# Kernel tuning notes

Hardware: AMD Instinct MI355X
Metric: run time of the kernel (lower is better)

## Reference

```python
import jax, jax.numpy as jnp
import numpy as np

N = 100000
E = 3200000
D = 128


def setup_inputs() -> dict:
    key = jax.random.key(0)
    k1, k2, k3, k4 = jax.random.split(key, 4)
    x = jax.random.normal(k1, (N, D), dtype=jnp.float32)
    edge_index = jax.random.randint(k2, (2, E), 0, N, dtype=jnp.int64)
    W1 = jax.random.normal(k3, (D, 16), dtype=jnp.float32) * (1.0 / np.sqrt(D))
    b1 = jnp.zeros((16,), dtype=jnp.float32)
    W2 = jax.random.normal(k4, (16, 2), dtype=jnp.float32) * (1.0 / np.sqrt(16))
    b2 = jnp.zeros((2,), dtype=jnp.float32)
    return {"x": x, "edge_index": edge_index, "W1": W1, "b1": b1, "W2": W2, "b2": b2}


def _gcn_conv(h, src, dst, norm, W, b):
    # transform first (out_dim <= in_dim), then normalized scatter-add aggregation
    h = h @ W                                   # [N, out]
    msg = h[src] * norm[:, None]                # [E+N, out] gathered messages
    agg = jax.ops.segment_sum(msg, dst, num_segments=N)
    return agg + b


def reference(x, edge_index, W1, b1, W2, b2):
    loops = jnp.arange(N, dtype=edge_index.dtype)
    src = jnp.concatenate([edge_index[0], loops])   # row (message source)
    dst = jnp.concatenate([edge_index[1], loops])   # col (aggregation target)
    # symmetric GCN normalization: deg over dst, norm = d^-1/2[src] * d^-1/2[dst]
    deg = jax.ops.segment_sum(jnp.ones_like(src, dtype=x.dtype), dst, num_segments=N)
    dinv = jnp.where(deg > 0, jax.lax.rsqrt(deg), 0.0)
    norm = dinv[src] * dinv[dst]

    h = _gcn_conv(x, src, dst, norm, W1, b1)
    h = jax.nn.relu(h)
    h = _gcn_conv(h, src, dst, norm, W2, b2)
    return jax.nn.log_softmax(h, axis=1)
```

## Files before the change

### kernel.cpp

```cpp
#include <hip/hip_runtime.h>
#include <hip/hip_fp16.h>
#include <math.h>

#define N_NODES 100000
#define N_EDGES 3200000
#define D_IN    128
#define H1      16

#define BSH     8
#define NPB     256
#define NB      391
#define CAP     13056
#define PBLK    512
#define CHUNK   6250
#define ELS_CAP 12128
#define NLINES  (ELS_CAP / 16)
#define MROWS   64
#define SLOTS   26
#define AELS    5120


__global__ __launch_bounds__(512) void k_zero(int* __restrict__ cursor) {
    int t = threadIdx.x;
    if (t < NB) cursor[t] = 0;
}

__global__ __launch_bounds__(512) void k_partition(const int* __restrict__ ei,
                                                   int* __restrict__ cursor,
                                                   unsigned int* __restrict__ eop) {
    __shared__ int h[512];
    __shared__ int loff[512];
    __shared__ int resv[NB];
    __shared__ unsigned short owner[NLINES];
    __shared__ unsigned char rank8[CHUNK];
    __shared__ unsigned int els[ELS_CAP];
    int t = threadIdx.x;
    h[t] = 0;
    __syncthreads();
    int c0 = blockIdx.x * CHUNK;
    const int* srcs = ei + c0;
    const int* dsts = ei + N_EDGES + c0;
    for (int i = t; i < CHUNK; i += 512)
        rank8[i] = (unsigned char)atomicAdd(&h[dsts[i] >> BSH], 1);
    __syncthreads();
    int cp = (h[t] + 15) & ~15;
    loff[t] = cp;
    __syncthreads();
    for (int o = 1; o < 512; o <<= 1) {
        int u = (t >= o) ? loff[t - o] : 0;
        __syncthreads();
        loff[t] += u;
        __syncthreads();
    }
    int inc = loff[t];
    int totalpad = loff[511];
    int ex = inc - cp;
    __syncthreads();
    loff[t] = ex;
    if (t < NB && cp) {
        resv[t] = atomicAdd(&cursor[t], cp);
        int l0 = ex >> 4;
        for (int k = 0; k < (cp >> 4); ++k) owner[l0 + k] = (unsigned short)t;
    }
    for (int i = t; i < totalpad; i += 512) els[i] = 0xFFFFFFFFu;
    __syncthreads();
    for (int i = t; i < CHUNK; i += 512) {
        int s = srcs[i];
        int d = dsts[i];
        int b = d >> BSH;
        els[loff[b] + (int)rank8[i]] = ((unsigned)s << BSH) | (unsigned)(d & (NPB - 1));
    }
    __syncthreads();
    for (int i = t; i < totalpad; i += 512) {
        int b   = owner[i >> 4];
        int pos = resv[b] + (i - loff[b]);
        if (pos < CAP)
            eop[(size_t)b * CAP + pos] = els[i];
    }
}

__global__ __launch_bounds__(512) void k_count(const int* __restrict__ cursor,
                                               const unsigned int* __restrict__ eop,
                                               float* __restrict__ dinv) {
    __shared__ int cnt[128];
    int t = threadIdx.x;
    int b = blockIdx.x >> 1, hh = blockIdx.x & 1;
    if (t < 128) cnt[t] = 0;
    __syncthreads();
    int n = cursor[b]; if (n > CAP) n = CAP;
    const unsigned int* reg = eop + (size_t)b * CAP;
    for (int i = t; i < n; i += 512) {
        unsigned int v = reg[i];
        if ((int)v >= 0) {
            int dloc = v & (NPB - 1);
            if ((dloc >> 7) == hh) atomicAdd(&cnt[dloc & 127], 1);
        }
    }
    __syncthreads();
    if (t < 128) {
        int node = (b << BSH) + (hh << 7) + t;
        if (node < N_NODES) dinv[node] = rsqrtf((float)(cnt[t] + 1));
    }
}

__global__ __launch_bounds__(256) void k_mm1(const float* __restrict__ x,
                                             const float* __restrict__ W1,
                                             const float* __restrict__ dinv,
                                             __half* __restrict__ h1h) {
    __shared__ float sX[MROWS][D_IN + 1];
    int t = threadIdx.x;
    int r0 = blockIdx.x * MROWS;
    for (int i = t; i < MROWS * (D_IN / 4); i += 256) {
        int row = i >> 5, c4 = i & 31;
        int grow = r0 + row;
        float4 v = (grow < N_NODES) ? ((const float4*)x)[(size_t)grow * 32 + c4]
                                    : make_float4(0.f, 0.f, 0.f, 0.f);
        sX[row][c4 * 4 + 0] = v.x; sX[row][c4 * 4 + 1] = v.y;
        sX[row][c4 * 4 + 2] = v.z; sX[row][c4 * 4 + 3] = v.w;
    }
    __syncthreads();
    int lane = t & 63;
    int c0 = __builtin_amdgcn_readfirstlane((t >> 6) * 4);
    float a0 = 0.f, a1 = 0.f, a2 = 0.f, a3 = 0.f;
#pragma unroll 4
    for (int d = 0; d < D_IN; ++d) {
        float xv = sX[lane][d];
        a0 = fmaf(xv, W1[d * 16 + c0 + 0], a0);
        a1 = fmaf(xv, W1[d * 16 + c0 + 1], a1);
        a2 = fmaf(xv, W1[d * 16 + c0 + 2], a2);
        a3 = fmaf(xv, W1[d * 16 + c0 + 3], a3);
    }
    int grow = r0 + lane;
    if (grow < N_NODES) {
        float di = dinv[grow];
        __half2* o = (__half2*)(h1h + (size_t)grow * H1 + c0);
        o[0] = __floats2half2_rn(a0 * di, a1 * di);
        o[1] = __floats2half2_rn(a2 * di, a3 * di);
    }
}

__global__ __launch_bounds__(512) void k_agg1f(const int* __restrict__ cursor,
                                               const unsigned int* __restrict__ eop,
                                               const __half* __restrict__ h1h,
                                               const float* __restrict__ dinv,
                                               const float* __restrict__ b1,
                                               const float* __restrict__ W2,
                                               float2* __restrict__ h2f) {
    __shared__ int cnt[128], off[128];
    __shared__ int els[AELS];
    int t = threadIdx.x;
    int b = blockIdx.x >> 1, hh = blockIdx.x & 1;
    if (t < 128) cnt[t] = 0;
    __syncthreads();
    int n = cursor[b]; if (n > CAP) n = CAP;
    const unsigned int* reg = eop + (size_t)b * CAP;
    unsigned int vals[SLOTS];
#pragma unroll
    for (int k = 0; k < SLOTS; ++k) {
        int i = t + k * 512;
        unsigned int w = 0xFFFFFFFFu;
        if (i < n) {
            unsigned int v = reg[i];
            if ((int)v >= 0) {
                int dloc = v & (NPB - 1);
                if ((dloc >> 7) == hh) {
                    int r = atomicAdd(&cnt[dloc & 127], 1);
                    w = (v >> 8) | ((unsigned)(r & 127) << 17)
                                 | ((unsigned)(dloc & 127) << 24);
                }
            }
        }
        vals[k] = w;
    }
    __syncthreads();
    int val = (t < 128) ? cnt[t] : 0;
    if (t < 128) off[t] = val;
    __syncthreads();
    for (int o = 1; o < 128; o <<= 1) {
        int u = 0;
        if (t < 128 && t >= o) u = off[t - o];
        __syncthreads();
        if (t < 128) off[t] += u;
        __syncthreads();
    }
    if (t < 128) off[t] -= val;
    __syncthreads();
#pragma unroll
    for (int k = 0; k < SLOTS; ++k) {
        unsigned int w = vals[k];
        if (w != 0xFFFFFFFFu) {
            int src  = w & 0x1FFFF;
            int r    = (w >> 17) & 127;
            int dloc = (w >> 24) & 127;
            int p = off[dloc] + r;
            if (p < AELS) els[p] = src;
        }
    }
    __syncthreads();
    int g = t >> 4, l = t & 15;
    for (int nn = g; nn < 128; nn += 32) {
        int node = (b << BSH) + (hh << 7) + nn;
        if (node >= N_NODES) continue;
        int e = cnt[nn], base = off[nn];
        float acc = 0.f;
        int j = 0;
        for (; j + 4 <= e; j += 4) {
            int s0 = els[base + j],     s1 = els[base + j + 1];
            int s2 = els[base + j + 2], s3 = els[base + j + 3];
            acc += __half2float(h1h[s0 * H1 + l]) + __half2float(h1h[s1 * H1 + l])
                 + __half2float(h1h[s2 * H1 + l]) + __half2float(h1h[s3 * H1 + l]);
        }
        for (; j < e; ++j) acc += __half2float(h1h[els[base + j] * H1 + l]);
        float di = dinv[node];
        float s  = acc + __half2float(h1h[node * H1 + l]);
        float h  = fmaxf(fmaf(di, s, b1[l]), 0.f);
        float p0 = h * W2[2 * l], p1 = h * W2[2 * l + 1];
#pragma unroll
        for (int o2 = 1; o2 < 16; o2 <<= 1) {
            p0 += __shfl_xor(p0, o2);
            p1 += __shfl_xor(p1, o2);
        }
        if (l == 0) h2f[node] = make_float2(p0 * di, p1 * di);
    }
}

__global__ __launch_bounds__(512) void k_agg2f(const int* __restrict__ cursor,
                                               const unsigned int* __restrict__ eop,
                                               const float2* __restrict__ h2f,
                                               const float* __restrict__ dinv,
                                               const float* __restrict__ b2,
                                               float* __restrict__ out) {
    __shared__ float ax[128], ay[128];
    int t = threadIdx.x;
    int b = blockIdx.x >> 1, hh = blockIdx.x & 1;
    if (t < 128) { ax[t] = 0.f; ay[t] = 0.f; }
    __syncthreads();
    int n = cursor[b]; if (n > CAP) n = CAP;
    const unsigned int* reg = eop + (size_t)b * CAP;
    for (int i = t; i < n; i += 512) {
        unsigned int v = reg[i];
        if ((int)v >= 0) {
            int dloc = v & (NPB - 1);
            if ((dloc >> 7) == hh) {
                float2 m = h2f[v >> 8];
                atomicAdd(&ax[dloc & 127], m.x);
                atomicAdd(&ay[dloc & 127], m.y);
            }
        }
    }
    __syncthreads();
    if (t < 128) {
        int node = (b << BSH) + (hh << 7) + t;
        if (node < N_NODES) {
            float di = dinv[node];
            float2 self = h2f[node];
            float a0 = fmaf(di, ax[t] + self.x, b2[0]);
            float a1 = fmaf(di, ay[t] + self.y, b2[1]);
            float m  = fmaxf(a0, a1);
            float lg = logf(expf(a0 - m) + expf(a1 - m));
            out[2 * node]     = a0 - m - lg;
            out[2 * node + 1] = a1 - m - lg;
        }
    }
}

extern "C" void kernel_launch(void* const* d_in, const int* in_sizes, int n_in,
                              void* d_out, int out_size, void* d_ws, size_t ws_size,
                              hipStream_t stream) {
    const float* x  = (const float*)d_in[0];
    const int*   ei = (const int*)d_in[1];
    const float* W1 = (const float*)d_in[2];
    const float* b1 = (const float*)d_in[3];
    const float* W2 = (const float*)d_in[4];
    const float* b2 = (const float*)d_in[5];
    float* out = (float*)d_out;

    int*          cursor = (int*)d_ws;
    float*        dinv   = (float*)(cursor + 512);
    __half*       h1h    = (__half*)(dinv + 100352);
    float2*       h2f    = (float2*)(h1h + (size_t)100352 * H1);
    unsigned int* eop    = (unsigned int*)(h2f + 100352);

    k_zero     <<<1,      512, 0, stream>>>(cursor);
    k_partition<<<PBLK,   512, 0, stream>>>(ei, cursor, eop);
    k_count    <<<NB * 2, 512, 0, stream>>>(cursor, eop, dinv);
    k_mm1      <<<(N_NODES + MROWS - 1) / MROWS, 256, 0, stream>>>(x, W1, dinv, h1h);
    k_agg1f    <<<NB * 2, 512, 0, stream>>>(cursor, eop, h1h, dinv, b1, W2, h2f);
    k_agg2f    <<<NB * 2, 512, 0, stream>>>(cursor, eop, h2f, dinv, b2, out);
}
```

Baseline: 248.2 us.

## Precompute per-node CSR offsets in k_count and vectorize edge and feature gathers

k_count now also runs a per-half-bucket prefix scan and writes each node's degree and offset to global buffers. k_agg1f reads these instead of re-counting and re-scanning, scattering sources directly into shared memory through per-node atomic cursors and dropping the 26-slot register staging array. All edge-stream loops read the partitioned edge list as uint4, and layer-1 aggregation uses 4 threads per node, each loading 4 halves at once, instead of 16 threads loading one half each. This adds two global arrays and relies on each bucket's edge count being a multiple of 4.

```diff
diff --git a/kernel.cpp b/kernel.cpp
--- a/kernel.cpp
+++ b/kernel.cpp
@@ -16,9 +16,10 @@
 #define ELS_CAP 12128
 #define NLINES  (ELS_CAP / 16)
 #define MROWS   64
-#define SLOTS   26
 #define AELS    5120
 
+
+union H4 { uint2 u; __half2 h[2]; };
 
 __global__ __launch_bounds__(512) void k_zero(int* __restrict__ cursor) {
     int t = threadIdx.x;
@@ -81,25 +82,39 @@
 
 __global__ __launch_bounds__(512) void k_count(const int* __restrict__ cursor,
                                                const unsigned int* __restrict__ eop,
-                                               float* __restrict__ dinv) {
-    __shared__ int cnt[128];
+                                               float* __restrict__ dinv,
+                                               int* __restrict__ gdeg,
+                                               int* __restrict__ goff) {
+    __shared__ int cnt[128], off[128];
     int t = threadIdx.x;
     int b = blockIdx.x >> 1, hh = blockIdx.x & 1;
     if (t < 128) cnt[t] = 0;
     __syncthreads();
     int n = cursor[b]; if (n > CAP) n = CAP;
-    const unsigned int* reg = eop + (size_t)b * CAP;
-    for (int i = t; i < n; i += 512) {
-        unsigned int v = reg[i];
-        if ((int)v >= 0) {
-            int dloc = v & (NPB - 1);
-            if ((dloc >> 7) == hh) atomicAdd(&cnt[dloc & 127], 1);
-        }
-    }
-    __syncthreads();
+    const uint4* reg4 = (const uint4*)(eop + (size_t)b * CAP);
+    for (int i = t; i < (n >> 2); i += 512) {
+        uint4 v = reg4[i];
+        if ((int)v.x >= 0 && (((v.x & (NPB-1)) >> 7) == (unsigned)hh)) atomicAdd(&cnt[v.x & 127], 1);
+        if ((int)v.y >= 0 && (((v.y & (NPB-1)) >> 7) == (unsigned)hh)) atomicAdd(&cnt[v.y & 127], 1);
+        if ((int)v.z >= 0 && (((v.z & (NPB-1)) >> 7) == (unsigned)hh)) atomicAdd(&cnt[v.z & 127], 1);
+        if ((int)v.w >= 0 && (((v.w & (NPB-1)) >> 7) == (unsigned)hh)) atomicAdd(&cnt[v.w & 127], 1);
+    }
+    __syncthreads();
+    int val = (t < 128) ? cnt[t] : 0;
+    if (t < 128) off[t] = val;
+    __syncthreads();
+    for (int o = 1; o < 128; o <<= 1) {
+        int u = 0;
+        if (t < 128 && t >= o) u = off[t - o];
+        __syncthreads();
+        if (t < 128) off[t] += u;
+        __syncthreads();
+    }
     if (t < 128) {
         int node = (b << BSH) + (hh << 7) + t;
-        if (node < N_NODES) dinv[node] = rsqrtf((float)(cnt[t] + 1));
+        if (node < N_NODES) dinv[node] = rsqrtf((float)(val + 1));
+        gdeg[blockIdx.x * 128 + t] = val;
+        goff[blockIdx.x * 128 + t] = off[t] - val;
     }
 }
 
@@ -141,87 +156,78 @@
 
 __global__ __launch_bounds__(512) void k_agg1f(const int* __restrict__ cursor,
                                                const unsigned int* __restrict__ eop,
+                                               const int* __restrict__ gdeg,
+                                               const int* __restrict__ goff,
                                                const __half* __restrict__ h1h,
                                                const float* __restrict__ dinv,
                                                const float* __restrict__ b1,
                                                const float* __restrict__ W2,
                                                float2* __restrict__ h2f) {
-    __shared__ int cnt[128], off[128];
+    __shared__ int cnt[128], off[128], cur[128];
     __shared__ int els[AELS];
     int t = threadIdx.x;
     int b = blockIdx.x >> 1, hh = blockIdx.x & 1;
-    if (t < 128) cnt[t] = 0;
+    if (t < 128) {
+        int c = gdeg[blockIdx.x * 128 + t];
+        int o = goff[blockIdx.x * 128 + t];
+        cnt[t] = c; off[t] = o; cur[t] = o;
+    }
     __syncthreads();
     int n = cursor[b]; if (n > CAP) n = CAP;
-    const unsigned int* reg = eop + (size_t)b * CAP;
-    unsigned int vals[SLOTS];
+    const uint4* reg4 = (const uint4*)(eop + (size_t)b * CAP);
+    for (int i = t; i < (n >> 2); i += 512) {
+        uint4 v = reg4[i];
 #pragma unroll
-    for (int k = 0; k < SLOTS; ++k) {
-        int i = t + k * 512;
-        unsigned int w = 0xFFFFFFFFu;
-        if (i < n) {
-            unsigned int v = reg[i];
-            if ((int)v >= 0) {
-                int dloc = v & (NPB - 1);
+        for (int k = 0; k < 4; ++k) {
+            unsigned int w = (k == 0) ? v.x : (k == 1) ? v.y : (k == 2) ? v.z : v.w;
+            if ((int)w >= 0) {
+                int dloc = w & (NPB - 1);
                 if ((dloc >> 7) == hh) {
-                    int r = atomicAdd(&cnt[dloc & 127], 1);
-                    w = (v >> 8) | ((unsigned)(r & 127) << 17)
-                                 | ((unsigned)(dloc & 127) << 24);
+                    int r = atomicAdd(&cur[dloc & 127], 1);
+                    if (r < AELS) els[r] = w >> 8;
                 }
             }
         }
-        vals[k] = w;
-    }
-    __syncthreads();
-    int val = (t < 128) ? cnt[t] : 0;
-    if (t < 128) off[t] = val;
-    __syncthreads();
-    for (int o = 1; o < 128; o <<= 1) {
-        int u = 0;
-        if (t < 128 && t >= o) u = off[t - o];
-        __syncthreads();
-        if (t < 128) off[t] += u;
-        __syncthreads();
-    }
-    if (t < 128) off[t] -= val;
-    __syncthreads();
-#pragma unroll
-    for (int k = 0; k < SLOTS; ++k) {
-        unsigned int w = vals[k];
-        if (w != 0xFFFFFFFFu) {
-            int src  = w & 0x1FFFF;
-            int r    = (w >> 17) & 127;
-            int dloc = (w >> 24) & 127;
-            int p = off[dloc] + r;
-            if (p < AELS) els[p] = src;
-        }
-    }
-    __syncthreads();
-    int g = t >> 4, l = t & 15;
-    for (int nn = g; nn < 128; nn += 32) {
-        int node = (b << BSH) + (hh << 7) + nn;
-        if (node >= N_NODES) continue;
-        int e = cnt[nn], base = off[nn];
-        float acc = 0.f;
-        int j = 0;
-        for (; j + 4 <= e; j += 4) {
-            int s0 = els[base + j],     s1 = els[base + j + 1];
-            int s2 = els[base + j + 2], s3 = els[base + j + 3];
-            acc += __half2float(h1h[s0 * H1 + l]) + __half2float(h1h[s1 * H1 + l])
-                 + __half2float(h1h[s2 * H1 + l]) + __half2float(h1h[s3 * H1 + l]);
-        }
-        for (; j < e; ++j) acc += __half2float(h1h[els[base + j] * H1 + l]);
-        float di = dinv[node];
-        float s  = acc + __half2float(h1h[node * H1 + l]);
-        float h  = fmaxf(fmaf(di, s, b1[l]), 0.f);
-        float p0 = h * W2[2 * l], p1 = h * W2[2 * l + 1];
-#pragma unroll
-        for (int o2 = 1; o2 < 16; o2 <<= 1) {
-            p0 += __shfl_xor(p0, o2);
-            p1 += __shfl_xor(p1, o2);
-        }
-        if (l == 0) h2f[node] = make_float2(p0 * di, p1 * di);
-    }
+    }
+    __syncthreads();
+    int g = t >> 2, l = t & 3;
+    int node = (b << BSH) + (hh << 7) + g;
+    if (node >= N_NODES) return;
+    int e = cnt[g], base = off[g];
+    float a0 = 0.f, a1 = 0.f, a2 = 0.f, a3 = 0.f;
+    int j = 0;
+    for (; j + 4 <= e; j += 4) {
+        int s0 = els[base + j],     s1 = els[base + j + 1];
+        int s2 = els[base + j + 2], s3 = els[base + j + 3];
+        H4 m0, m1, m2, m3;
+        m0.u = ((const uint2*)(h1h + s0 * H1))[l];
+        m1.u = ((const uint2*)(h1h + s1 * H1))[l];
+        m2.u = ((const uint2*)(h1h + s2 * H1))[l];
+        m3.u = ((const uint2*)(h1h + s3 * H1))[l];
+        a0 += __low2float(m0.h[0]) + __low2float(m1.h[0]) + __low2float(m2.h[0]) + __low2float(m3.h[0]);
+        a1 += __high2float(m0.h[0]) + __high2float(m1.h[0]) + __high2float(m2.h[0]) + __high2float(m3.h[0]);
+        a2 += __low2float(m0.h[1]) + __low2float(m1.h[1]) + __low2float(m2.h[1]) + __low2float(m3.h[1]);
+        a3 += __high2float(m0.h[1]) + __high2float(m1.h[1]) + __high2float(m2.h[1]) + __high2float(m3.h[1]);
+    }
+    for (; j < e; ++j) {
+        H4 m; m.u = ((const uint2*)(h1h + els[base + j] * H1))[l];
+        a0 += __low2float(m.h[0]); a1 += __high2float(m.h[0]);
+        a2 += __low2float(m.h[1]); a3 += __high2float(m.h[1]);
+    }
+    H4 sf; sf.u = ((const uint2*)(h1h + node * H1))[l];
+    a0 += __low2float(sf.h[0]); a1 += __high2float(sf.h[0]);
+    a2 += __low2float(sf.h[1]); a3 += __high2float(sf.h[1]);
+    float di = dinv[node];
+    int f = 4 * l;
+    float h0 = fmaxf(fmaf(di, a0, b1[f + 0]), 0.f);
+    float h1v = fmaxf(fmaf(di, a1, b1[f + 1]), 0.f);
+    float h2 = fmaxf(fmaf(di, a2, b1[f + 2]), 0.f);
+    float h3 = fmaxf(fmaf(di, a3, b1[f + 3]), 0.f);
+    float p0 = h0 * W2[2*f] + h1v * W2[2*f+2] + h2 * W2[2*f+4] + h3 * W2[2*f+6];
+    float p1 = h0 * W2[2*f+1] + h1v * W2[2*f+3] + h2 * W2[2*f+5] + h3 * W2[2*f+7];
+    p0 += __shfl_xor(p0, 1); p1 += __shfl_xor(p1, 1);
+    p0 += __shfl_xor(p0, 2); p1 += __shfl_xor(p1, 2);
+    if (l == 0) h2f[node] = make_float2(p0 * di, p1 * di);
 }
 
 __global__ __launch_bounds__(512) void k_agg2f(const int* __restrict__ cursor,
@@ -236,15 +242,19 @@
     if (t < 128) { ax[t] = 0.f; ay[t] = 0.f; }
     __syncthreads();
     int n = cursor[b]; if (n > CAP) n = CAP;
-    const unsigned int* reg = eop + (size_t)b * CAP;
-    for (int i = t; i < n; i += 512) {
-        unsigned int v = reg[i];
-        if ((int)v >= 0) {
-            int dloc = v & (NPB - 1);
-            if ((dloc >> 7) == hh) {
-                float2 m = h2f[v >> 8];
-                atomicAdd(&ax[dloc & 127], m.x);
-                atomicAdd(&ay[dloc & 127], m.y);
+    const uint4* reg4 = (const uint4*)(eop + (size_t)b * CAP);
+    for (int i = t; i < (n >> 2); i += 512) {
+        uint4 v = reg4[i];
+#pragma unroll
+        for (int k = 0; k < 4; ++k) {
+            unsigned int w = (k == 0) ? v.x : (k == 1) ? v.y : (k == 2) ? v.z : v.w;
+            if ((int)w >= 0) {
+                int dloc = w & (NPB - 1);
+                if ((dloc >> 7) == hh) {
+                    float2 m = h2f[w >> 8];
+                    atomicAdd(&ax[dloc & 127], m.x);
+                    atomicAdd(&ay[dloc & 127], m.y);
+                }
             }
         }
     }
@@ -277,14 +287,16 @@
 
     int*          cursor = (int*)d_ws;
     float*        dinv   = (float*)(cursor + 512);
-    __half*       h1h    = (__half*)(dinv + 100352);
+    int*          gdeg   = (int*)(dinv + 100352);
+    int*          goff   = gdeg + 100352;
+    __half*       h1h    = (__half*)(goff + 100352);
     float2*       h2f    = (float2*)(h1h + (size_t)100352 * H1);
     unsigned int* eop    = (unsigned int*)(h2f + 100352);
 
     k_zero     <<<1,      512, 0, stream>>>(cursor);
     k_partition<<<PBLK,   512, 0, stream>>>(ei, cursor, eop);
-    k_count    <<<NB * 2, 512, 0, stream>>>(cursor, eop, dinv);
+    k_count    <<<NB * 2, 512, 0, stream>>>(cursor, eop, dinv, gdeg, goff);
     k_mm1      <<<(N_NODES + MROWS - 1) / MROWS, 256, 0, stream>>>(x, W1, dinv, h1h);
-    k_agg1f    <<<NB * 2, 512, 0, stream>>>(cursor, eop, h1h, dinv, b1, W2, h2f);
+    k_agg1f    <<<NB * 2, 512, 0, stream>>>(cursor, eop, gdeg, goff, h1h, dinv, b1, W2, h2f);
     k_agg2f    <<<NB * 2, 512, 0, stream>>>(cursor, eop, h2f, dinv, b2, out);
 }
```

Result: faster. 225.0 us (-9.3%).
